# Kernel tuning notes

Measured on AMD Instinct MI355X. Metric: run time of the kernel, lower is better.

The kernel has to match this reference:

```python
import jax, jax.numpy as jnp
import numpy as np

H_SIZE = 1024
N_HEADS = 16
D_K = H_SIZE // N_HEADS


def setup_inputs() -> dict:
    key = jax.random.key(0)
    ks = jax.random.split(key, 12)
    s = 1.0 / np.sqrt(H_SIZE)
    inp = {
        "x": jax.random.normal(ks[0], (2, 2048, H_SIZE), dtype=jnp.float32),
        "Wq": jax.random.uniform(ks[1], (H_SIZE, H_SIZE), minval=-s, maxval=s),
        "bq": jax.random.uniform(ks[2], (H_SIZE,), minval=-s, maxval=s),
        "Wk": jax.random.uniform(ks[3], (H_SIZE, H_SIZE), minval=-s, maxval=s),
        "bk": jax.random.uniform(ks[4], (H_SIZE,), minval=-s, maxval=s),
        "Wv": jax.random.uniform(ks[5], (H_SIZE, H_SIZE), minval=-s, maxval=s),
        "bv": jax.random.uniform(ks[6], (H_SIZE,), minval=-s, maxval=s),
        "Wo": jax.random.uniform(ks[7], (H_SIZE, H_SIZE), minval=-s, maxval=s),
        "bo": jax.random.uniform(ks[8], (H_SIZE,), minval=-s, maxval=s),
        "ln_gamma": jnp.ones((H_SIZE,), dtype=jnp.float32),
        "ln_beta": jnp.zeros((H_SIZE,), dtype=jnp.float32),
    }
    return inp


def reference(x, Wq, bq, Wk, bk, Wv, bv, Wo, bo, ln_gamma, ln_beta):
    B, L, H = x.shape
    residual = x
    # QKV projections -> [B, n_heads, L, d_k]
    def proj(W, b):
        return (x @ W.T + b).reshape(B, L, N_HEADS, D_K).transpose(0, 2, 1, 3)
    q = proj(Wq, bq)
    k = proj(Wk, bk)
    v = proj(Wv, bv)
    # scaled dot-product attention (dropout = identity in eval mode)
    scores = jnp.einsum("bhqd,bhkd->bhqk", q, k) / jnp.sqrt(jnp.float32(D_K))
    attn = jax.nn.softmax(scores, axis=-1)
    out = jnp.einsum("bhqk,bhkd->bhqd", attn, v)
    out = out.transpose(0, 2, 1, 3).reshape(B, L, H)
    out = out @ Wo.T + bo
    # residual + LayerNorm
    y = out + residual
    mu = jnp.mean(y, axis=-1, keepdims=True)
    var = jnp.var(y, axis=-1, keepdims=True)
    y = (y - mu) / jnp.sqrt(var + 1e-5) * ln_gamma + ln_beta
    return y
```

## Files before the change

kernel.cpp:

```cpp
#include <hip/hip_runtime.h>

#define H_SIZE 1024
#define N_HEADS 16
#define D_K 64
#define SEQ 2048
#define BATCH 2
#define M_TOT 4096

typedef __bf16 __attribute__((ext_vector_type(8))) bf16_8;
typedef float __attribute__((ext_vector_type(4))) f32x4;
typedef float __attribute__((ext_vector_type(16))) f32x16;
typedef int __attribute__((ext_vector_type(4))) int4v;

#define SWZ(r) ((((r) & 7) ^ (((r) >> 3) & 7)))

__device__ __forceinline__ ushort f2bf(float f) {
    unsigned int u = __float_as_uint(f);
    unsigned int r = (u + 0x7FFFu + ((u >> 16) & 1u)) >> 16;
    return (ushort)r;
}

__device__ __forceinline__ unsigned int cvtpk(float lo, float hi) {
    unsigned int r;
    asm("v_cvt_pk_bf16_f32 %0, %1, %2" : "=v"(r) : "v"(lo), "v"(hi));
    return r;
}

__device__ __forceinline__ float exp2_raw(float x) {
    float r;
    asm("v_exp_f32 %0, %1" : "=v"(r) : "v"(x));
    return r;
}

__device__ __forceinline__ void gld16(void* lds, const void* g) {
    __builtin_amdgcn_global_load_lds(
        (const __attribute__((address_space(1))) unsigned int*)g,
        (__attribute__((address_space(3))) unsigned int*)lds, 16, 0, 0);
}

__global__ __launch_bounds__(256) void cast_all_kernel(
    const float* __restrict__ x, const float* __restrict__ wq, const float* __restrict__ wk,
    const float* __restrict__ wv, const float* __restrict__ wo,
    ushort* __restrict__ xb, ushort* __restrict__ wqb, ushort* __restrict__ wkb,
    ushort* __restrict__ wvb, ushort* __restrict__ wob) {
    int i = blockIdx.x * 256 + threadIdx.x;
    const float* src;
    ushort* dst;
    int off;
    if (i < 1048576) {
        src = x; dst = xb; off = i;
    } else {
        int j = i - 1048576;
        int w = j >> 18;
        off = j & 262143;
        src = (w == 0) ? wq : (w == 1) ? wk : (w == 2) ? wv : wo;
        dst = (w == 0) ? wqb : (w == 1) ? wkb : (w == 2) ? wvb : wob;
    }
    float4 v = ((const float4*)src)[off];
    ushort4 o;
    o.x = f2bf(v.x); o.y = f2bf(v.y); o.z = f2bf(v.z); o.w = f2bf(v.w);
    ((ushort4*)dst)[off] = o;
}

__global__ __launch_bounds__(256) void gemm_qkv(
    const ushort* __restrict__ A, const ushort* __restrict__ wq,
    const ushort* __restrict__ wk, const ushort* __restrict__ wv,
    const float* __restrict__ bq, const float* __restrict__ bk, const float* __restrict__ bv,
    ushort* __restrict__ Qb, ushort* __restrict__ Kb, ushort* __restrict__ Vtb) {
    constexpr int BK = 32;
    __shared__ ushort As[3][128 * BK];
    __shared__ ushort Bs[3][128 * BK];
    const int tid = threadIdx.x;
    const int lane = tid & 63, wid = tid >> 6;
    const int wr = wid >> 1, wc = wid & 1;
    const int hi = lane >> 4, lo = lane & 15;
    const int bm0 = blockIdx.x * 128;
    const int t3 = blockIdx.y >> 3;
    const int bn0 = (blockIdx.y & 7) * 128;
    const ushort* Bw = (t3 == 0) ? wq : (t3 == 1) ? wk : wv;
    const float* bias = (t3 == 0) ? bq : (t3 == 1) ? bk : bv;

    f32x4 acc[4][4] = {};

    const int srow = tid >> 2;
    const int sseg = ((tid & 3) ^ ((tid >> 3) & 3)) * 8;
    const ushort* gaB = A + (size_t)(bm0 + srow) * H_SIZE + sseg;
    const ushort* gbB = Bw + (size_t)(bn0 + srow) * H_SIZE + sseg;
    const int ldsOff = tid * 16;

#define STAGE(ba, bb, kt)                                 \
    {                                                     \
        char* la = (char*)(ba) + ldsOff;                  \
        char* lb = (char*)(bb) + ldsOff;                  \
        gld16(la, gaB + (kt));                            \
        gld16(la + 4096, gaB + 64 * H_SIZE + (kt));       \
        gld16(lb, gbB + (kt));                            \
        gld16(lb + 4096, gbB + 64 * H_SIZE + (kt));       \
    }

    STAGE(&As[0][0], &Bs[0][0], 0);
    STAGE(&As[1][0], &Bs[1][0], BK);
    asm volatile("s_waitcnt vmcnt(4)" ::: "memory");
    __builtin_amdgcn_s_barrier();
    __builtin_amdgcn_sched_barrier(0);

    constexpr int NT = H_SIZE / BK;
    const int rxv = (lo >> 1) & 3;
    int cur = 0;
    for (int t = 0; t < NT; t++) {
        int c2 = cur + 2; if (c2 >= 3) c2 -= 3;
        if (t + 2 < NT) STAGE(&As[c2][0], &Bs[c2][0], (t + 2) * BK);
        {
            bf16_8 af[4], bfv[4];
            const ushort* pa = &As[cur][(wr * 64 + lo) * BK + ((hi ^ rxv) * 8)];
            const ushort* pb = &Bs[cur][(wc * 64 + lo) * BK + ((hi ^ rxv) * 8)];
#pragma unroll
            for (int i = 0; i < 4; i++) af[i] = *(const bf16_8*)(pa + i * 16 * BK);
#pragma unroll
            for (int i = 0; i < 4; i++) bfv[i] = *(const bf16_8*)(pb + i * 16 * BK);
#pragma unroll
            for (int mi = 0; mi < 4; mi++)
#pragma unroll
                for (int ni = 0; ni < 4; ni++)
                    acc[mi][ni] = __builtin_amdgcn_mfma_f32_16x16x32_bf16(
                        af[mi], bfv[ni], acc[mi][ni], 0, 0, 0);
        }
        if (t + 1 < NT) {
            if (t + 2 < NT) { asm volatile("s_waitcnt vmcnt(4)" ::: "memory"); }
            else            { asm volatile("s_waitcnt vmcnt(0)" ::: "memory"); }
            __builtin_amdgcn_s_barrier();
            __builtin_amdgcn_sched_barrier(0);
        }
        cur = cur + 1; if (cur >= 3) cur -= 3;
    }
#undef STAGE

#pragma unroll
    for (int mi = 0; mi < 4; mi++) {
#pragma unroll
        for (int ni = 0; ni < 4; ni++) {
            const int row0 = bm0 + wr * 64 + mi * 16 + hi * 4;
            const int col = bn0 + wc * 64 + ni * 16 + lo;
            const float bv = bias[col];
            const int h = col >> 6, dk = col & 63;
            if (t3 == 2) {
                const int b = row0 >> 11, l0 = row0 & 2047;
                const int lsw0 = (l0 & ~63) | (((((l0 >> 3) & 7) ^ SWZ(dk)) & 7) << 3) | (l0 & 7);
                uint2 o;
                o.x = cvtpk(acc[mi][ni][0] + bv, acc[mi][ni][1] + bv);
                o.y = cvtpk(acc[mi][ni][2] + bv, acc[mi][ni][3] + bv);
                *(uint2*)&Vtb[((size_t)(b * N_HEADS + h) * D_K + dk) * SEQ + lsw0] = o;
            } else {
#pragma unroll
                for (int rr = 0; rr < 4; rr++) {
                    const int m = row0 + rr;
                    const int b = m >> 11, l = m & 2047;
                    float val = acc[mi][ni][rr] + bv;
                    if (t3 == 0) {
                        Qb[((size_t)(b * N_HEADS + h) * SEQ + l) * D_K + dk] =
                            f2bf(val * 0.18033688f);
                    } else {
                        int dks = ((((dk >> 3) ^ SWZ(l & 63)) & 7) << 3) | (dk & 7);
                        Kb[((size_t)(b * N_HEADS + h) * SEQ + l) * D_K + dks] = f2bf(val);
                    }
                }
            }
        }
    }
}

__global__ __launch_bounds__(256) void gemm_o(const ushort* __restrict__ A,
                                              const ushort* __restrict__ Bw,
                                              const float* __restrict__ bias,
                                              const float* __restrict__ resid,
                                              float* __restrict__ outp) {
    constexpr int BK = 32;
    __shared__ ushort As[3][128 * BK];
    __shared__ ushort Bs[3][64 * BK];
    const int tid = threadIdx.x;
    const int lane = tid & 63, wid = tid >> 6;
    const int wr = wid >> 1, wc = wid & 1;
    const int hi = lane >> 4, lo = lane & 15;
    const int bm0 = blockIdx.x * 128, bn0 = blockIdx.y * 64;

    f32x4 acc[4][2] = {};

    const int srow = tid >> 2;
    const int sseg = ((tid & 3) ^ ((tid >> 3) & 3)) * 8;
    const ushort* gaB = A + (size_t)(bm0 + srow) * H_SIZE + sseg;
    const ushort* gbB = Bw + (size_t)(bn0 + srow) * H_SIZE + sseg;
    const int ldsOff = tid * 16;

#define STAGE(ba, bb, kt)                                 \
    {                                                     \
        char* la = (char*)(ba) + ldsOff;                  \
        gld16(la, gaB + (kt));                            \
        gld16(la + 4096, gaB + 64 * H_SIZE + (kt));       \
        gld16((char*)(bb) + ldsOff, gbB + (kt));          \
    }

    STAGE(&As[0][0], &Bs[0][0], 0);
    STAGE(&As[1][0], &Bs[1][0], BK);
    asm volatile("s_waitcnt vmcnt(3)" ::: "memory");
    __builtin_amdgcn_s_barrier();
    __builtin_amdgcn_sched_barrier(0);

    constexpr int NT = H_SIZE / BK;
    const int rxv = (lo >> 1) & 3;
    int cur = 0;
    for (int t = 0; t < NT; t++) {
        int c2 = cur + 2; if (c2 >= 3) c2 -= 3;
        if (t + 2 < NT) STAGE(&As[c2][0], &Bs[c2][0], (t + 2) * BK);
        {
            bf16_8 af[4], bfv[2];
            const ushort* pa = &As[cur][(wr * 64 + lo) * BK + ((hi ^ rxv) * 8)];
            const ushort* pb = &Bs[cur][(wc * 32 + lo) * BK + ((hi ^ rxv) * 8)];
#pragma unroll
            for (int i = 0; i < 4; i++) af[i] = *(const bf16_8*)(pa + i * 16 * BK);
#pragma unroll
            for (int i = 0; i < 2; i++) bfv[i] = *(const bf16_8*)(pb + i * 16 * BK);
#pragma unroll
            for (int mi = 0; mi < 4; mi++)
#pragma unroll
                for (int ni = 0; ni < 2; ni++)
                    acc[mi][ni] = __builtin_amdgcn_mfma_f32_16x16x32_bf16(
                        af[mi], bfv[ni], acc[mi][ni], 0, 0, 0);
        }
        if (t + 1 < NT) {
            if (t + 2 < NT) { asm volatile("s_waitcnt vmcnt(3)" ::: "memory"); }
            else            { asm volatile("s_waitcnt vmcnt(0)" ::: "memory"); }
            __builtin_amdgcn_s_barrier();
            __builtin_amdgcn_sched_barrier(0);
        }
        cur = cur + 1; if (cur >= 3) cur -= 3;
    }
#undef STAGE

#pragma unroll
    for (int mi = 0; mi < 4; mi++) {
#pragma unroll
        for (int ni = 0; ni < 2; ni++) {
            const int row0 = bm0 + wr * 64 + mi * 16 + hi * 4;
            const int col = bn0 + wc * 32 + ni * 16 + lo;
            const float bv = bias[col];
#pragma unroll
            for (int rr = 0; rr < 4; rr++) {
                const int m = row0 + rr;
                outp[(size_t)m * H_SIZE + col] =
                    acc[mi][ni][rr] + bv + resid[(size_t)m * H_SIZE + col];
            }
        }
    }
}

__global__ __launch_bounds__(256) void attn_kernel(const ushort* __restrict__ Q,
                                                   const ushort* __restrict__ Ksw,
                                                   const ushort* __restrict__ Vsw,
                                                   ushort* __restrict__ Out) {
    __shared__ ushort Ks[2][64 * 64];
    __shared__ ushort Vs[2][64 * 64];
    __shared__ float lsum_lds[4][32];
    const int lane = threadIdx.x & 63, wid = threadIdx.x >> 6;
    const int h32 = lane >> 5, q32 = lane & 31;
    const int bh = blockIdx.y;
    const int q0w = blockIdx.x * 128 + wid * 32;
    const ushort* Qh = Q + (size_t)bh * SEQ * D_K;
    const ushort* Kp = Ksw + (size_t)bh * SEQ * D_K;
    const ushort* Vp = Vsw + (size_t)bh * D_K * SEQ;

    bf16_8 qf[4];
#pragma unroll
    for (int tt = 0; tt < 4; tt++)
        qf[tt] = *(const bf16_8*)(Qh + (size_t)(q0w + q32) * D_K + tt * 16 + h32 * 8);

    f32x16 oacc0 = {}, oacc1 = {};
    float ls = 0.f;

    const int koff = wid * 2048 + lane * 16;
    const int vrow = wid * 16 + (lane >> 3);
    const int vseg = (lane & 7) * 16;

#define STAGE(bb, kt)                                                             \
    {                                                                             \
        const char* kg = (const char*)(Kp + (size_t)(kt) * D_K);                  \
        char* kl = (char*)&Ks[bb][0];                                             \
        gld16(kl + koff, kg + koff);                                              \
        gld16(kl + koff + 1024, kg + koff + 1024);                                \
        char* vl = (char*)&Vs[bb][0];                                             \
        gld16(vl + vrow * 128 + vseg,                                             \
              (const char*)(Vp + (size_t)vrow * SEQ + (kt)) + vseg);              \
        gld16(vl + (vrow + 8) * 128 + vseg,                                       \
              (const char*)(Vp + (size_t)(vrow + 8) * SEQ + (kt)) + vseg);        \
    }

    STAGE(0, 0);
    __syncthreads();
    int buf = 0;
    for (int t = 0; t < SEQ / 64; t++) {
        if (t + 1 < SEQ / 64) STAGE(buf ^ 1, (t + 1) * 64);
        const ushort* kb = &Ks[buf][0];
        const ushort* vb = &Vs[buf][0];
#pragma unroll
        for (int kh = 0; kh < 2; kh++) {
            f32x16 st = {};
            const int krow = kh * 32 + q32;
#pragma unroll
            for (int tt = 0; tt < 4; tt++) {
                int sg = (2 * tt + h32) ^ SWZ(krow);
                bf16_8 kf = *(const bf16_8*)(kb + krow * 64 + sg * 8);
                st = __builtin_amdgcn_mfma_f32_32x32x16_bf16(kf, qf[tt], st, 0, 0, 0);
            }
            float p[16];
#pragma unroll
            for (int rr = 0; rr < 16; rr++) p[rr] = exp2_raw(st[rr]);
            float partial = 0.f;
#pragma unroll
            for (int rr = 0; rr < 16; rr++) partial += p[rr];
            ls += partial + __shfl_xor(partial, 32);

            union { unsigned int w[4]; bf16_8 v; } pf0, pf1;
#pragma unroll
            for (int i = 0; i < 2; i++) {
                unsigned int a = cvtpk(p[2 * i], p[2 * i + 1]);
                unsigned int b = cvtpk(p[4 + 2 * i], p[4 + 2 * i + 1]);
                asm volatile("v_permlane32_swap_b32 %0, %1" : "+v"(a), "+v"(b));
                pf0.w[i] = a; pf0.w[2 + i] = b;
                unsigned int c = cvtpk(p[8 + 2 * i], p[8 + 2 * i + 1]);
                unsigned int d = cvtpk(p[12 + 2 * i], p[12 + 2 * i + 1]);
                asm volatile("v_permlane32_swap_b32 %0, %1" : "+v"(c), "+v"(d));
                pf1.w[i] = c; pf1.w[2 + i] = d;
            }

            {
                const int vr0 = q32;
                int sg0 = (4 * kh + h32) ^ SWZ(vr0);
                int sg1 = (4 * kh + 2 + h32) ^ SWZ(vr0);
                bf16_8 vf0 = *(const bf16_8*)(vb + vr0 * 64 + sg0 * 8);
                bf16_8 vf1 = *(const bf16_8*)(vb + vr0 * 64 + sg1 * 8);
                oacc0 = __builtin_amdgcn_mfma_f32_32x32x16_bf16(pf0.v, vf0, oacc0, 0, 0, 0);
                oacc0 = __builtin_amdgcn_mfma_f32_32x32x16_bf16(pf1.v, vf1, oacc0, 0, 0, 0);
            }
            {
                const int vr1 = 32 + q32;
                int sg0 = (4 * kh + h32) ^ SWZ(vr1);
                int sg1 = (4 * kh + 2 + h32) ^ SWZ(vr1);
                bf16_8 vf0 = *(const bf16_8*)(vb + vr1 * 64 + sg0 * 8);
                bf16_8 vf1 = *(const bf16_8*)(vb + vr1 * 64 + sg1 * 8);
                oacc1 = __builtin_amdgcn_mfma_f32_32x32x16_bf16(pf0.v, vf0, oacc1, 0, 0, 0);
                oacc1 = __builtin_amdgcn_mfma_f32_32x32x16_bf16(pf1.v, vf1, oacc1, 0, 0, 0);
            }
        }
        __syncthreads();
        buf ^= 1;
    }
#undef STAGE

    if (lane < 32) lsum_lds[wid][q32] = 1.0f / ls;
    const int b = bh >> 4, h = bh & 15;
#pragma unroll
    for (int rr = 0; rr < 16; rr++) {
        const int qloc = (rr & 3) + 8 * (rr >> 2) + 4 * h32;
        const float inv = lsum_lds[wid][qloc];
        const int l = q0w + qloc;
        ushort* orow = Out + ((size_t)(b * SEQ + l)) * H_SIZE + h * 64;
        orow[q32] = f2bf(oacc0[rr] * inv);
        orow[32 + q32] = f2bf(oacc1[rr] * inv);
    }
}

__global__ __launch_bounds__(256) void ln_kernel(float* __restrict__ y,
                                                 const float* __restrict__ gamma,
                                                 const float* __restrict__ beta) {
    const int row = blockIdx.x;
    float4* p = (float4*)(y + (size_t)row * H_SIZE);
    float4 v = p[threadIdx.x];
    float s = v.x + v.y + v.z + v.w;
    float s2 = v.x * v.x + v.y * v.y + v.z * v.z + v.w * v.w;
#pragma unroll
    for (int off = 1; off < 64; off <<= 1) {
        s += __shfl_xor(s, off);
        s2 += __shfl_xor(s2, off);
    }
    __shared__ float ss[4], ss2[4];
    const int wid = threadIdx.x >> 6, lane = threadIdx.x & 63;
    if (lane == 0) { ss[wid] = s; ss2[wid] = s2; }
    __syncthreads();
    s = ss[0] + ss[1] + ss[2] + ss[3];
    s2 = ss2[0] + ss2[1] + ss2[2] + ss2[3];
    const float mean = s * (1.0f / H_SIZE);
    const float var = s2 * (1.0f / H_SIZE) - mean * mean;
    const float rstd = rsqrtf(var + 1e-5f);
    const float4 g = ((const float4*)gamma)[threadIdx.x];
    const float4 bt = ((const float4*)beta)[threadIdx.x];
    float4 o;
    o.x = (v.x - mean) * rstd * g.x + bt.x;
    o.y = (v.y - mean) * rstd * g.y + bt.y;
    o.z = (v.z - mean) * rstd * g.z + bt.z;
    o.w = (v.w - mean) * rstd * g.w + bt.w;
    p[threadIdx.x] = o;
}

extern "C" void kernel_launch(void* const* d_in, const int* in_sizes, int n_in,
                              void* d_out, int out_size, void* d_ws, size_t ws_size,
                              hipStream_t stream) {
    const float* x = (const float*)d_in[0];
    const float* Wq = (const float*)d_in[1];
    const float* bq = (const float*)d_in[2];
    const float* Wk = (const float*)d_in[3];
    const float* bk = (const float*)d_in[4];
    const float* Wv = (const float*)d_in[5];
    const float* bv = (const float*)d_in[6];
    const float* Wo = (const float*)d_in[7];
    const float* bo = (const float*)d_in[8];
    const float* gamma = (const float*)d_in[9];
    const float* beta = (const float*)d_in[10];

    char* ws = (char*)d_ws;
    ushort* xb  = (ushort*)(ws);
    ushort* wqb = (ushort*)(ws + (8u << 20));
    ushort* wkb = (ushort*)(ws + (10u << 20));
    ushort* wvb = (ushort*)(ws + (12u << 20));
    ushort* wob = (ushort*)(ws + (14u << 20));
    ushort* Qb  = (ushort*)(ws + (16u << 20));
    ushort* Kb  = (ushort*)(ws + (24u << 20));
    ushort* Vtb = (ushort*)(ws + (32u << 20));
    ushort* Ao  = (ushort*)(ws + (40u << 20));

    cast_all_kernel<<<8192, 256, 0, stream>>>(x, Wq, Wk, Wv, Wo, xb, wqb, wkb, wvb, wob);

    dim3 gq(M_TOT / 128, 24);
    gemm_qkv<<<gq, 256, 0, stream>>>(xb, wqb, wkb, wvb, bq, bk, bv, Qb, Kb, Vtb);

    dim3 g2(SEQ / 128, BATCH * N_HEADS);
    attn_kernel<<<g2, 256, 0, stream>>>(Qb, Kb, Vtb, Ao);

    dim3 go(M_TOT / 128, H_SIZE / 64);
    gemm_o<<<go, 256, 0, stream>>>(Ao, wob, bo, x, (float*)d_out);

    ln_kernel<<<M_TOT, 256, 0, stream>>>((float*)d_out, gamma, beta);
}
```

Baseline: 136.2 us.

## Split attention along KV into two halves and merge with combine kernel

Attention grid gains a z dimension that splits the key sequence in two, doubling block count from 512 to 1024 to raise CU occupancy. Each half writes unnormalized bf16 outputs and row sums, and a new combine kernel adds them and normalizes. Row sums are now computed with an MFMA against a ones vector instead of VALU adds and shuffles, and s_setprio hints are placed around MFMA sections. This costs an extra launch, extra global traffic for partials, and bf16 rounding of unnormalized partial outputs. Softmax has no max subtraction, so summing the two halves directly is valid.

```diff
diff --git a/kernel.cpp b/kernel.cpp
--- a/kernel.cpp
+++ b/kernel.cpp
@@ -256,14 +256,17 @@
 __global__ __launch_bounds__(256) void attn_kernel(const ushort* __restrict__ Q,
                                                    const ushort* __restrict__ Ksw,
                                                    const ushort* __restrict__ Vsw,
-                                                   ushort* __restrict__ Out) {
+                                                   ushort* __restrict__ Op0,
+                                                   ushort* __restrict__ Op1,
+                                                   float* __restrict__ Lpart) {
     __shared__ ushort Ks[2][64 * 64];
     __shared__ ushort Vs[2][64 * 64];
-    __shared__ float lsum_lds[4][32];
     const int lane = threadIdx.x & 63, wid = threadIdx.x >> 6;
     const int h32 = lane >> 5, q32 = lane & 31;
     const int bh = blockIdx.y;
+    const int z = blockIdx.z;
     const int q0w = blockIdx.x * 128 + wid * 32;
+    const int kbase = z * (SEQ / 2);
     const ushort* Qh = Q + (size_t)bh * SEQ * D_K;
     const ushort* Kp = Ksw + (size_t)bh * SEQ * D_K;
     const ushort* Vp = Vsw + (size_t)bh * D_K * SEQ;
@@ -273,8 +276,11 @@
     for (int tt = 0; tt < 4; tt++)
         qf[tt] = *(const bf16_8*)(Qh + (size_t)(q0w + q32) * D_K + tt * 16 + h32 * 8);
 
-    f32x16 oacc0 = {}, oacc1 = {};
-    float ls = 0.f;
+    bf16_8 onesf;
+#pragma unroll
+    for (int i = 0; i < 8; i++) onesf[i] = (__bf16)1.0f;
+
+    f32x16 oacc0 = {}, oacc1 = {}, lsacc = {};
 
     const int koff = wid * 2048 + lane * 16;
     const int vrow = wid * 16 + (lane >> 3);
@@ -293,30 +299,29 @@
               (const char*)(Vp + (size_t)(vrow + 8) * SEQ + (kt)) + vseg);        \
     }
 
-    STAGE(0, 0);
+    STAGE(0, kbase);
     __syncthreads();
     int buf = 0;
-    for (int t = 0; t < SEQ / 64; t++) {
-        if (t + 1 < SEQ / 64) STAGE(buf ^ 1, (t + 1) * 64);
+    constexpr int NTT = (SEQ / 2) / 64;
+    for (int t = 0; t < NTT; t++) {
+        if (t + 1 < NTT) STAGE(buf ^ 1, kbase + (t + 1) * 64);
         const ushort* kb = &Ks[buf][0];
         const ushort* vb = &Vs[buf][0];
 #pragma unroll
         for (int kh = 0; kh < 2; kh++) {
             f32x16 st = {};
             const int krow = kh * 32 + q32;
+            __builtin_amdgcn_s_setprio(1);
 #pragma unroll
             for (int tt = 0; tt < 4; tt++) {
                 int sg = (2 * tt + h32) ^ SWZ(krow);
                 bf16_8 kf = *(const bf16_8*)(kb + krow * 64 + sg * 8);
                 st = __builtin_amdgcn_mfma_f32_32x32x16_bf16(kf, qf[tt], st, 0, 0, 0);
             }
+            __builtin_amdgcn_s_setprio(0);
             float p[16];
 #pragma unroll
             for (int rr = 0; rr < 16; rr++) p[rr] = exp2_raw(st[rr]);
-            float partial = 0.f;
-#pragma unroll
-            for (int rr = 0; rr < 16; rr++) partial += p[rr];
-            ls += partial + __shfl_xor(partial, 32);
 
             union { unsigned int w[4]; bf16_8 v; } pf0, pf1;
 #pragma unroll
@@ -331,6 +336,9 @@
                 pf1.w[i] = c; pf1.w[2 + i] = d;
             }
 
+            __builtin_amdgcn_s_setprio(1);
+            lsacc = __builtin_amdgcn_mfma_f32_32x32x16_bf16(pf0.v, onesf, lsacc, 0, 0, 0);
+            lsacc = __builtin_amdgcn_mfma_f32_32x32x16_bf16(pf1.v, onesf, lsacc, 0, 0, 0);
             {
                 const int vr0 = q32;
                 int sg0 = (4 * kh + h32) ^ SWZ(vr0);
@@ -349,23 +357,50 @@
                 oacc1 = __builtin_amdgcn_mfma_f32_32x32x16_bf16(pf0.v, vf0, oacc1, 0, 0, 0);
                 oacc1 = __builtin_amdgcn_mfma_f32_32x32x16_bf16(pf1.v, vf1, oacc1, 0, 0, 0);
             }
+            __builtin_amdgcn_s_setprio(0);
         }
         __syncthreads();
         buf ^= 1;
     }
 #undef STAGE
 
-    if (lane < 32) lsum_lds[wid][q32] = 1.0f / ls;
+    ushort* Op = (z == 0) ? Op0 : Op1;
+    float* Lp = Lpart + (size_t)z * N_HEADS * BATCH * SEQ;
     const int b = bh >> 4, h = bh & 15;
 #pragma unroll
     for (int rr = 0; rr < 16; rr++) {
         const int qloc = (rr & 3) + 8 * (rr >> 2) + 4 * h32;
-        const float inv = lsum_lds[wid][qloc];
         const int l = q0w + qloc;
-        ushort* orow = Out + ((size_t)(b * SEQ + l)) * H_SIZE + h * 64;
-        orow[q32] = f2bf(oacc0[rr] * inv);
-        orow[32 + q32] = f2bf(oacc1[rr] * inv);
-    }
+        ushort* orow = Op + ((size_t)(b * SEQ + l)) * H_SIZE + h * 64;
+        orow[q32] = f2bf(oacc0[rr]);
+        orow[32 + q32] = f2bf(oacc1[rr]);
+        if (q32 == 0) Lp[(size_t)bh * SEQ + l] = lsacc[rr];
+    }
+}
+
+__global__ __launch_bounds__(256) void combine_kernel(const ushort* __restrict__ O0,
+                                                      const ushort* __restrict__ O1,
+                                                      const float* __restrict__ Lp,
+                                                      ushort* __restrict__ Ao) {
+    int idx = blockIdx.x * 256 + threadIdx.x;
+    int m = idx >> 7;
+    int col0 = (idx & 127) * 8;
+    int b = m >> 11, l = m & 2047, h = col0 >> 6;
+    int bh = b * N_HEADS + h;
+    float inv = 1.0f / (Lp[(size_t)bh * SEQ + l] +
+                        Lp[(size_t)(N_HEADS * BATCH + bh) * SEQ + l]);
+    size_t off = (size_t)m * H_SIZE + col0;
+    int4v a = *(const int4v*)(O0 + off);
+    int4v c = *(const int4v*)(O1 + off);
+    unsigned int r[4];
+#pragma unroll
+    for (int j = 0; j < 4; j++) {
+        unsigned int ua = (unsigned int)a[j], uc = (unsigned int)c[j];
+        float lo = __uint_as_float(ua << 16) + __uint_as_float(uc << 16);
+        float hi = __uint_as_float(ua & 0xFFFF0000u) + __uint_as_float(uc & 0xFFFF0000u);
+        r[j] = cvtpk(lo * inv, hi * inv);
+    }
+    *(int4v*)(Ao + off) = *(const int4v*)r;
 }
 
 __global__ __launch_bounds__(256) void ln_kernel(float* __restrict__ y,
@@ -425,14 +460,19 @@
     ushort* Kb  = (ushort*)(ws + (24u << 20));
     ushort* Vtb = (ushort*)(ws + (32u << 20));
     ushort* Ao  = (ushort*)(ws + (40u << 20));
+    ushort* Op0 = (ushort*)(ws);
+    ushort* Op1 = Ao;
+    float*  Lpt = (float*)(ws + (48u << 20));
 
     cast_all_kernel<<<8192, 256, 0, stream>>>(x, Wq, Wk, Wv, Wo, xb, wqb, wkb, wvb, wob);
 
     dim3 gq(M_TOT / 128, 24);
     gemm_qkv<<<gq, 256, 0, stream>>>(xb, wqb, wkb, wvb, bq, bk, bv, Qb, Kb, Vtb);
 
-    dim3 g2(SEQ / 128, BATCH * N_HEADS);
-    attn_kernel<<<g2, 256, 0, stream>>>(Qb, Kb, Vtb, Ao);
+    dim3 g2(SEQ / 128, BATCH * N_HEADS, 2);
+    attn_kernel<<<g2, 256, 0, stream>>>(Qb, Kb, Vtb, Op0, Op1, Lpt);
+
+    combine_kernel<<<(M_TOT * H_SIZE / 8) / 256, 256, 0, stream>>>(Op0, Op1, Lpt, Ao);
 
     dim3 go(M_TOT / 128, H_SIZE / 64);
     gemm_o<<<go, 256, 0, stream>>>(Ao, wob, bo, x, (float*)d_out);
```

Result: slower. 142.4 us (+4.6%).

## Triple-buffer attention K/V tiles with vmcnt waits, block swizzle and MFMA priority

Applied to the files above, without the earlier changes.

The attention kernel moves from double to triple buffering of K/V tiles. It keeps two tiles of loads in flight, using explicit s_waitcnt vmcnt and raw barriers in place of __syncthreads. Both QK^T score MFMAs are issued up front, and each half's softmax is interleaved with the PV MFMAs, with s_setprio raised around MFMA bursts. The block index is remapped so neighbouring blocks spread across (b,h), aiming at better cache locality and more overlap, at the cost of more LDS per block and reliance on the exact count of outstanding loads.

```diff
diff --git a/kernel.cpp b/kernel.cpp
--- a/kernel.cpp
+++ b/kernel.cpp
@@ -257,13 +257,17 @@
                                                    const ushort* __restrict__ Ksw,
                                                    const ushort* __restrict__ Vsw,
                                                    ushort* __restrict__ Out) {
-    __shared__ ushort Ks[2][64 * 64];
-    __shared__ ushort Vs[2][64 * 64];
+    __shared__ ushort Ks[3][64 * 64];
+    __shared__ ushort Vs[3][64 * 64];
     __shared__ float lsum_lds[4][32];
     const int lane = threadIdx.x & 63, wid = threadIdx.x >> 6;
     const int h32 = lane >> 5, q32 = lane & 31;
-    const int bh = blockIdx.y;
-    const int q0w = blockIdx.x * 128 + wid * 32;
+
+    const int lin = blockIdx.y * gridDim.x + blockIdx.x;
+    const int nlin = (lin & 7) * 64 + (lin >> 3);
+    const int bx = nlin & 15;
+    const int bh = nlin >> 4;
+    const int q0 = bx * 128 + wid * 32;
     const ushort* Qh = Q + (size_t)bh * SEQ * D_K;
     const ushort* Kp = Ksw + (size_t)bh * SEQ * D_K;
     const ushort* Vp = Vsw + (size_t)bh * D_K * SEQ;
@@ -271,7 +275,7 @@
     bf16_8 qf[4];
 #pragma unroll
     for (int tt = 0; tt < 4; tt++)
-        qf[tt] = *(const bf16_8*)(Qh + (size_t)(q0w + q32) * D_K + tt * 16 + h32 * 8);
+        qf[tt] = *(const bf16_8*)(Qh + (size_t)(q0 + q32) * D_K + tt * 16 + h32 * 8);
 
     f32x16 oacc0 = {}, oacc1 = {};
     float ls = 0.f;
@@ -294,64 +298,116 @@
     }
 
     STAGE(0, 0);
-    __syncthreads();
-    int buf = 0;
-    for (int t = 0; t < SEQ / 64; t++) {
-        if (t + 1 < SEQ / 64) STAGE(buf ^ 1, (t + 1) * 64);
-        const ushort* kb = &Ks[buf][0];
-        const ushort* vb = &Vs[buf][0];
-#pragma unroll
-        for (int kh = 0; kh < 2; kh++) {
-            f32x16 st = {};
-            const int krow = kh * 32 + q32;
-#pragma unroll
-            for (int tt = 0; tt < 4; tt++) {
-                int sg = (2 * tt + h32) ^ SWZ(krow);
-                bf16_8 kf = *(const bf16_8*)(kb + krow * 64 + sg * 8);
-                st = __builtin_amdgcn_mfma_f32_32x32x16_bf16(kf, qf[tt], st, 0, 0, 0);
-            }
-            float p[16];
-#pragma unroll
-            for (int rr = 0; rr < 16; rr++) p[rr] = exp2_raw(st[rr]);
-            float partial = 0.f;
-#pragma unroll
-            for (int rr = 0; rr < 16; rr++) partial += p[rr];
-            ls += partial + __shfl_xor(partial, 32);
-
-            union { unsigned int w[4]; bf16_8 v; } pf0, pf1;
-#pragma unroll
-            for (int i = 0; i < 2; i++) {
-                unsigned int a = cvtpk(p[2 * i], p[2 * i + 1]);
-                unsigned int b = cvtpk(p[4 + 2 * i], p[4 + 2 * i + 1]);
-                asm volatile("v_permlane32_swap_b32 %0, %1" : "+v"(a), "+v"(b));
-                pf0.w[i] = a; pf0.w[2 + i] = b;
-                unsigned int c = cvtpk(p[8 + 2 * i], p[8 + 2 * i + 1]);
-                unsigned int d = cvtpk(p[12 + 2 * i], p[12 + 2 * i + 1]);
-                asm volatile("v_permlane32_swap_b32 %0, %1" : "+v"(c), "+v"(d));
-                pf1.w[i] = c; pf1.w[2 + i] = d;
-            }
-
-            {
-                const int vr0 = q32;
-                int sg0 = (4 * kh + h32) ^ SWZ(vr0);
-                int sg1 = (4 * kh + 2 + h32) ^ SWZ(vr0);
-                bf16_8 vf0 = *(const bf16_8*)(vb + vr0 * 64 + sg0 * 8);
-                bf16_8 vf1 = *(const bf16_8*)(vb + vr0 * 64 + sg1 * 8);
-                oacc0 = __builtin_amdgcn_mfma_f32_32x32x16_bf16(pf0.v, vf0, oacc0, 0, 0, 0);
-                oacc0 = __builtin_amdgcn_mfma_f32_32x32x16_bf16(pf1.v, vf1, oacc0, 0, 0, 0);
-            }
-            {
-                const int vr1 = 32 + q32;
-                int sg0 = (4 * kh + h32) ^ SWZ(vr1);
-                int sg1 = (4 * kh + 2 + h32) ^ SWZ(vr1);
-                bf16_8 vf0 = *(const bf16_8*)(vb + vr1 * 64 + sg0 * 8);
-                bf16_8 vf1 = *(const bf16_8*)(vb + vr1 * 64 + sg1 * 8);
-                oacc1 = __builtin_amdgcn_mfma_f32_32x32x16_bf16(pf0.v, vf0, oacc1, 0, 0, 0);
-                oacc1 = __builtin_amdgcn_mfma_f32_32x32x16_bf16(pf1.v, vf1, oacc1, 0, 0, 0);
-            }
-        }
-        __syncthreads();
-        buf ^= 1;
+    STAGE(1, 64);
+    asm volatile("s_waitcnt vmcnt(4)" ::: "memory");
+    __builtin_amdgcn_s_barrier();
+    __builtin_amdgcn_sched_barrier(0);
+
+    constexpr int NTT = SEQ / 64;
+    int cur = 0;
+    for (int t = 0; t < NTT; t++) {
+        int c2 = cur + 2; if (c2 >= 3) c2 -= 3;
+        if (t + 2 < NTT) STAGE(c2, (t + 2) * 64);
+        const ushort* kb = &Ks[cur][0];
+        const ushort* vb = &Vs[cur][0];
+
+        f32x16 st0 = {}, st1 = {};
+        __builtin_amdgcn_s_setprio(1);
+#pragma unroll
+        for (int tt = 0; tt < 4; tt++) {
+            const int krow = q32;
+            int sg = (2 * tt + h32) ^ SWZ(krow);
+            bf16_8 kf = *(const bf16_8*)(kb + krow * 64 + sg * 8);
+            st0 = __builtin_amdgcn_mfma_f32_32x32x16_bf16(kf, qf[tt], st0, 0, 0, 0);
+        }
+#pragma unroll
+        for (int tt = 0; tt < 4; tt++) {
+            const int krow = 32 + q32;
+            int sg = (2 * tt + h32) ^ SWZ(krow);
+            bf16_8 kf = *(const bf16_8*)(kb + krow * 64 + sg * 8);
+            st1 = __builtin_amdgcn_mfma_f32_32x32x16_bf16(kf, qf[tt], st1, 0, 0, 0);
+        }
+        __builtin_amdgcn_s_setprio(0);
+
+        union { unsigned int w[4]; bf16_8 v; } pf00, pf01;
+        float part0 = 0.f;
+#pragma unroll
+        for (int rr = 0; rr < 16; rr++) { st0[rr] = exp2_raw(st0[rr]); part0 += st0[rr]; }
+#pragma unroll
+        for (int i = 0; i < 2; i++) {
+            unsigned int a = cvtpk(st0[2 * i], st0[2 * i + 1]);
+            unsigned int b = cvtpk(st0[4 + 2 * i], st0[4 + 2 * i + 1]);
+            asm volatile("v_permlane32_swap_b32 %0, %1" : "+v"(a), "+v"(b));
+            pf00.w[i] = a; pf00.w[2 + i] = b;
+            unsigned int c = cvtpk(st0[8 + 2 * i], st0[8 + 2 * i + 1]);
+            unsigned int d = cvtpk(st0[12 + 2 * i], st0[12 + 2 * i + 1]);
+            asm volatile("v_permlane32_swap_b32 %0, %1" : "+v"(c), "+v"(d));
+            pf01.w[i] = c; pf01.w[2 + i] = d;
+        }
+        ls += part0 + __shfl_xor(part0, 32);
+
+        __builtin_amdgcn_s_setprio(1);
+        {
+            const int vr0 = q32;
+            int sg0 = (h32) ^ SWZ(vr0);
+            int sg1 = (2 + h32) ^ SWZ(vr0);
+            bf16_8 vf0 = *(const bf16_8*)(vb + vr0 * 64 + sg0 * 8);
+            bf16_8 vf1 = *(const bf16_8*)(vb + vr0 * 64 + sg1 * 8);
+            oacc0 = __builtin_amdgcn_mfma_f32_32x32x16_bf16(pf00.v, vf0, oacc0, 0, 0, 0);
+            oacc0 = __builtin_amdgcn_mfma_f32_32x32x16_bf16(pf01.v, vf1, oacc0, 0, 0, 0);
+            const int vr1 = 32 + q32;
+            int sg2 = (h32) ^ SWZ(vr1);
+            int sg3 = (2 + h32) ^ SWZ(vr1);
+            bf16_8 vf2 = *(const bf16_8*)(vb + vr1 * 64 + sg2 * 8);
+            bf16_8 vf3 = *(const bf16_8*)(vb + vr1 * 64 + sg3 * 8);
+            oacc1 = __builtin_amdgcn_mfma_f32_32x32x16_bf16(pf00.v, vf2, oacc1, 0, 0, 0);
+            oacc1 = __builtin_amdgcn_mfma_f32_32x32x16_bf16(pf01.v, vf3, oacc1, 0, 0, 0);
+        }
+        __builtin_amdgcn_s_setprio(0);
+
+        union { unsigned int w[4]; bf16_8 v; } pf10, pf11;
+        float part1 = 0.f;
+#pragma unroll
+        for (int rr = 0; rr < 16; rr++) { st1[rr] = exp2_raw(st1[rr]); part1 += st1[rr]; }
+#pragma unroll
+        for (int i = 0; i < 2; i++) {
+            unsigned int a = cvtpk(st1[2 * i], st1[2 * i + 1]);
+            unsigned int b = cvtpk(st1[4 + 2 * i], st1[4 + 2 * i + 1]);
+            asm volatile("v_permlane32_swap_b32 %0, %1" : "+v"(a), "+v"(b));
+            pf10.w[i] = a; pf10.w[2 + i] = b;
+            unsigned int c = cvtpk(st1[8 + 2 * i], st1[8 + 2 * i + 1]);
+            unsigned int d = cvtpk(st1[12 + 2 * i], st1[12 + 2 * i + 1]);
+            asm volatile("v_permlane32_swap_b32 %0, %1" : "+v"(c), "+v"(d));
+            pf11.w[i] = c; pf11.w[2 + i] = d;
+        }
+        ls += part1 + __shfl_xor(part1, 32);
+
+        __builtin_amdgcn_s_setprio(1);
+        {
+            const int vr0 = q32;
+            int sg0 = (4 + h32) ^ SWZ(vr0);
+            int sg1 = (6 + h32) ^ SWZ(vr0);
+            bf16_8 vf0 = *(const bf16_8*)(vb + vr0 * 64 + sg0 * 8);
+            bf16_8 vf1 = *(const bf16_8*)(vb + vr0 * 64 + sg1 * 8);
+            oacc0 = __builtin_amdgcn_mfma_f32_32x32x16_bf16(pf10.v, vf0, oacc0, 0, 0, 0);
+            oacc0 = __builtin_amdgcn_mfma_f32_32x32x16_bf16(pf11.v, vf1, oacc0, 0, 0, 0);
+            const int vr1 = 32 + q32;
+            int sg2 = (4 + h32) ^ SWZ(vr1);
+            int sg3 = (6 + h32) ^ SWZ(vr1);
+            bf16_8 vf2 = *(const bf16_8*)(vb + vr1 * 64 + sg2 * 8);
+            bf16_8 vf3 = *(const bf16_8*)(vb + vr1 * 64 + sg3 * 8);
+            oacc1 = __builtin_amdgcn_mfma_f32_32x32x16_bf16(pf10.v, vf2, oacc1, 0, 0, 0);
+            oacc1 = __builtin_amdgcn_mfma_f32_32x32x16_bf16(pf11.v, vf3, oacc1, 0, 0, 0);
+        }
+        __builtin_amdgcn_s_setprio(0);
+
+        if (t + 1 < NTT) {
+            if (t + 2 < NTT) { asm volatile("s_waitcnt vmcnt(4)" ::: "memory"); }
+            else             { asm volatile("s_waitcnt vmcnt(0)" ::: "memory"); }
+            __builtin_amdgcn_s_barrier();
+            __builtin_amdgcn_sched_barrier(0);
+        }
+        cur = cur + 1; if (cur >= 3) cur -= 3;
     }
 #undef STAGE
 
@@ -361,7 +417,7 @@
     for (int rr = 0; rr < 16; rr++) {
         const int qloc = (rr & 3) + 8 * (rr >> 2) + 4 * h32;
         const float inv = lsum_lds[wid][qloc];
-        const int l = q0w + qloc;
+        const int l = q0 + qloc;
         ushort* orow = Out + ((size_t)(b * SEQ + l)) * H_SIZE + h * 64;
         orow[q32] = f2bf(oacc0[rr] * inv);
         orow[32 + q32] = f2bf(oacc1[rr] * inv);
```

Measured after the change: 136.3 us. Within noise of the previous version (+0.1%).
